# Performance work log

Measured on AMD Instinct MI355X. Metric: run time of the kernel, lower is better.

Reference implementation:

```python
import jax, jax.numpy as jnp
import numpy as np

B, K, E, L, H, ENS = 32768, 5, 16, 128, 3, 3

def setup_inputs() -> dict:
    key = jax.random.key(0)
    ks = jax.random.split(key, 16)
    w = lambda i, shape: (jax.random.normal(ks[i], shape, jnp.float32) * 0.05)
    return {
        "z": jax.random.normal(ks[0], (B, L), jnp.float32),
        "anchors": jax.random.normal(ks[1], (B, K, 2), jnp.float32),
        # anchor_embed MLP: Linear(2,E) -> ReLU -> Linear(E,E)
        "W1": w(2, (E, 2)), "b1": w(3, (E,)),
        "W2": w(4, (E, E)), "b2": w(5, (E,)),
        # LSTMCell(E, L): gates order i,f,g,o
        "W_ih": w(6, (4 * L, E)), "W_hh": w(7, (4 * L, L)),
        "b_ih": w(8, (4 * L,)), "b_hh": w(9, (4 * L,)),
        # progress head Linear(L,1)
        "Wp": w(10, (1, L)), "bp": w(11, (1,)),
        # risk ensemble: ENS stacked Linear(L,1)
        "Wr": w(12, (ENS, L)), "br": w(13, (ENS,)),
    }

def reference(z, anchors, W1, b1, W2, b2, W_ih, W_hh, b_ih, b_hh, Wp, bp, Wr, br):
    Bc, Kc, _ = anchors.shape
    # anchor embedding MLP (B,K,2) -> (B,K,E)
    emb = jnp.maximum(anchors @ W1.T + b1, 0.0) @ W2.T + b2
    inp = emb.reshape(Bc * Kc, -1)                      # (B*K, E)
    h = jnp.broadcast_to(z[:, None, :], (Bc, Kc, z.shape[-1])).reshape(Bc * Kc, -1)
    c = jnp.zeros_like(h)
    x_proj = inp @ W_ih.T + b_ih                        # input projection constant over steps
    for _ in range(H):  # fixed small rollout horizon
        gates = x_proj + h @ W_hh.T + b_hh              # (B*K, 4L)
        i_g, f_g, g_g, o_g = jnp.split(gates, 4, axis=-1)
        i_g = jax.nn.sigmoid(i_g)
        f_g = jax.nn.sigmoid(f_g)
        g_g = jnp.tanh(g_g)
        o_g = jax.nn.sigmoid(o_g)
        c = f_g * c + i_g * g_g
        h = o_g * jnp.tanh(c)
    h = h.reshape(Bc, Kc, -1)                           # (B,K,L)
    progress = (h @ Wp.T + bp)[..., 0]                  # (B,K)
    risks = jnp.einsum('bkl,el->ebk', h, Wr) + br[:, None, None]  # (ENS,B,K)
    risk_mean = risks.mean(axis=0)
    unc = jnp.var(jax.nn.sigmoid(risks), axis=0, ddof=1)  # torch .var is unbiased
    return risk_mean, progress, unc, risks
```

## Files before the change

### kernel.cpp

```cpp
#include <hip/hip_runtime.h>

#define BN 32768
#define KN 5
#define LN 128
#define EN 16
#define HN 3
#define ROWS (BN*KN)
#define BK (BN*KN)
#define MT 32
#define TILES (ROWS/MT)
#define WGS 512
#define TPW (TILES/WGS)
#define THREADS 512
#define ASTR 168
#define HSTR 132

using bf16x8 = __attribute__((ext_vector_type(8))) __bf16;
using f32x4  = __attribute__((ext_vector_type(4))) float;
using u16x8  = __attribute__((ext_vector_type(8))) unsigned short;

__device__ inline unsigned short f2bf(float x) {
    union { float f; unsigned u; } v; v.f = x;
    unsigned r = v.u + 0x7FFFu + ((v.u >> 16) & 1u);
    return (unsigned short)(r >> 16);
}
__device__ inline float sigm(float x) {
    return __builtin_amdgcn_rcpf(1.0f + __builtin_amdgcn_exp2f(-1.44269504089f * x));
}
__device__ inline float tanh_(float x) {
    return 1.0f - 2.0f * __builtin_amdgcn_rcpf(1.0f + __builtin_amdgcn_exp2f(2.88539008178f * x));
}
__device__ inline f32x4 splat4(float x) { f32x4 r; r[0]=x; r[1]=x; r[2]=x; r[3]=x; return r; }

__global__ __launch_bounds__(THREADS, 2)
void wahead_kernel(const float* __restrict__ z,   const float* __restrict__ anchors,
                   const float* __restrict__ W1,  const float* __restrict__ b1,
                   const float* __restrict__ W2,  const float* __restrict__ b2,
                   const float* __restrict__ Wih, const float* __restrict__ Whh,
                   const float* __restrict__ bih, const float* __restrict__ bhh,
                   const float* __restrict__ Wp,  const float* __restrict__ bp,
                   const float* __restrict__ Wr,  const float* __restrict__ br,
                   float* __restrict__ out)
{
    __shared__ unsigned short sA[2 * MT * ASTR];
    __shared__ float sHf[MT * HSTR];
    __shared__ float sW1[32], sb1[16], sW2[256], sb2[16], sWp[128], sWr[384];

    const int tid  = threadIdx.x;
    const int wv   = tid >> 6;
    const int lane = tid & 63;
    const int quad = lane >> 4;
    const int cc   = lane & 15;

    if (tid < 32)  sW1[tid] = W1[tid];
    if (tid < 16)  { sb1[tid] = b1[tid]; sb2[tid] = b2[tid]; }
    if (tid < 256) sW2[tid] = W2[tid];
    if (tid < 128) sWp[tid] = Wp[tid];
    if (tid < 384) sWr[tid] = Wr[tid];

    bf16x8 Bf[4][5];
    float biasv[4];
    #pragma unroll
    for (int t = 0; t < 4; ++t) {
        const int n = t * 128 + wv * 16 + cc;
        biasv[t] = bih[n] + bhh[n];
        #pragma unroll
        for (int kt = 0; kt < 5; ++kt) {
            const int k0 = kt * 32 + quad * 8;
            float v[8];
            if (k0 < 16) {
                const float4 p0 = *reinterpret_cast<const float4*>(Wih + n * 16 + k0);
                const float4 p1 = *reinterpret_cast<const float4*>(Wih + n * 16 + k0 + 4);
                v[0]=p0.x; v[1]=p0.y; v[2]=p0.z; v[3]=p0.w;
                v[4]=p1.x; v[5]=p1.y; v[6]=p1.z; v[7]=p1.w;
            } else if (k0 < 144) {
                const float4 p0 = *reinterpret_cast<const float4*>(Whh + n * 128 + (k0 - 16));
                const float4 p1 = *reinterpret_cast<const float4*>(Whh + n * 128 + (k0 - 16) + 4);
                v[0]=p0.x; v[1]=p0.y; v[2]=p0.z; v[3]=p0.w;
                v[4]=p1.x; v[5]=p1.y; v[6]=p1.z; v[7]=p1.w;
            } else {
                #pragma unroll
                for (int j = 0; j < 8; ++j) v[j] = 0.0f;
            }
            union { bf16x8 bv; unsigned short us[8]; } pk;
            #pragma unroll
            for (int j = 0; j < 8; ++j) pk.us[j] = f2bf(v[j]);
            Bf[t][kt] = pk.bv;
        }
    }

    const float bpv = bp[0];
    const float br0 = br[0], br1 = br[1], br2 = br[2];

    __syncthreads();

    const int erow = tid >> 4;
    const int esub = tid & 15;

    for (int ti = 0; ti < TPW; ++ti) {
        const int tile = blockIdx.x * TPW + ti;
        const int r0g  = tile * MT;

        {
            const int gr = r0g + erow;
            const float ax = anchors[gr * 2], ay = anchors[gr * 2 + 1];
            float acc_e = sb2[esub];
            #pragma unroll
            for (int hh = 0; hh < 16; ++hh) {
                float pre = fmaf(sW1[hh * 2], ax, fmaf(sW1[hh * 2 + 1], ay, sb1[hh]));
                pre = fmaxf(pre, 0.0f);
                acc_e = fmaf(pre, sW2[esub * 16 + hh], acc_e);
            }
            const unsigned short eb = f2bf(acc_e);
            sA[0 * MT * ASTR + erow * ASTR + esub] = eb;
            sA[1 * MT * ASTR + erow * ASTR + esub] = eb;
            sA[0 * MT * ASTR + erow * ASTR + 144 + esub] = 0;
            sA[1 * MT * ASTR + erow * ASTR + 144 + esub] = 0;
            const unsigned b_idx = (unsigned)gr / 5u;
            const float4* zp = reinterpret_cast<const float4*>(z + (size_t)b_idx * 128 + esub * 8);
            const float4 z0 = zp[0], z1 = zp[1];
            union { u16x8 v; unsigned short us[8]; } zz;
            zz.us[0]=f2bf(z0.x); zz.us[1]=f2bf(z0.y); zz.us[2]=f2bf(z0.z); zz.us[3]=f2bf(z0.w);
            zz.us[4]=f2bf(z1.x); zz.us[5]=f2bf(z1.y); zz.us[6]=f2bf(z1.z); zz.us[7]=f2bf(z1.w);
            *reinterpret_cast<u16x8*>(&sA[0 * MT * ASTR + erow * ASTR + 16 + esub * 8]) = zz.v;
        }

        float cst[2][4] = {{0,0,0,0},{0,0,0,0}};

        #pragma unroll
        for (int s = 0; s < HN; ++s) {
            const int cur = s & 1;
            const int nxt = cur ^ 1;
            __syncthreads();

            f32x4 acc[2][4];
            #pragma unroll
            for (int mt = 0; mt < 2; ++mt)
                #pragma unroll
                for (int t = 0; t < 4; ++t)
                    acc[mt][t] = splat4(biasv[t]);

            #pragma unroll
            for (int kt = 0; kt < 5; ++kt) {
                const bf16x8 a0 = *reinterpret_cast<const bf16x8*>(
                    &sA[cur * MT * ASTR + cc * ASTR + kt * 32 + quad * 8]);
                const bf16x8 a1 = *reinterpret_cast<const bf16x8*>(
                    &sA[cur * MT * ASTR + (16 + cc) * ASTR + kt * 32 + quad * 8]);
                #pragma unroll
                for (int t = 0; t < 4; ++t) {
                    acc[0][t] = __builtin_amdgcn_mfma_f32_16x16x32_bf16(a0, Bf[t][kt], acc[0][t], 0, 0, 0);
                    acc[1][t] = __builtin_amdgcn_mfma_f32_16x16x32_bf16(a1, Bf[t][kt], acc[1][t], 0, 0, 0);
                }
            }

            const int lcol = wv * 16 + cc;
            #pragma unroll
            for (int mt = 0; mt < 2; ++mt) {
                #pragma unroll
                for (int r = 0; r < 4; ++r) {
                    const float ig = sigm(acc[mt][0][r]);
                    const float fg = sigm(acc[mt][1][r]);
                    const float gg = tanh_(acc[mt][2][r]);
                    const float og = sigm(acc[mt][3][r]);
                    const float cn = fmaf(fg, cst[mt][r], ig * gg);
                    cst[mt][r] = cn;
                    const float hn = og * tanh_(cn);
                    const int m = mt * 16 + quad * 4 + r;
                    if (s == HN - 1) {
                        sHf[m * HSTR + lcol] = hn;
                    } else {
                        sA[nxt * MT * ASTR + m * ASTR + 16 + lcol] = f2bf(hn);
                    }
                }
            }
        }

        __syncthreads();

        {
            const int row = tid >> 4;
            const int j   = tid & 15;
            float p = 0.f, q0 = 0.f, q1 = 0.f, q2 = 0.f;
            #pragma unroll
            for (int u = 0; u < 8; ++u) {
                const int l = j * 8 + u;
                const float hv = sHf[row * HSTR + l];
                p  = fmaf(hv, sWp[l], p);
                q0 = fmaf(hv, sWr[l], q0);
                q1 = fmaf(hv, sWr[128 + l], q1);
                q2 = fmaf(hv, sWr[256 + l], q2);
            }
            #pragma unroll
            for (int m = 1; m < 16; m <<= 1) {
                p  += __shfl_xor(p,  m, 64);
                q0 += __shfl_xor(q0, m, 64);
                q1 += __shfl_xor(q1, m, 64);
                q2 += __shfl_xor(q2, m, 64);
            }
            if (j == 0) {
                const int gr = r0g + row;
                const float prog  = p + bpv;
                const float rr0 = q0 + br0, rr1 = q1 + br1, rr2 = q2 + br2;
                const float rmean = (rr0 + rr1 + rr2) * (1.0f / 3.0f);
                const float s0 = sigm(rr0), s1 = sigm(rr1), s2 = sigm(rr2);
                const float sm = (s0 + s1 + s2) * (1.0f / 3.0f);
                const float d0 = s0 - sm, d1 = s1 - sm, d2 = s2 - sm;
                const float unc = (d0 * d0 + d1 * d1 + d2 * d2) * 0.5f;
                out[gr]          = rmean;
                out[BK + gr]     = prog;
                out[2 * BK + gr] = unc;
                out[3 * BK + gr] = rr0;
                out[4 * BK + gr] = rr1;
                out[5 * BK + gr] = rr2;
            }
        }
    }
}

extern "C" void kernel_launch(void* const* d_in, const int* in_sizes, int n_in,
                              void* d_out, int out_size, void* d_ws, size_t ws_size,
                              hipStream_t stream) {
    const float* z       = (const float*)d_in[0];
    const float* anchors = (const float*)d_in[1];
    const float* W1      = (const float*)d_in[2];
    const float* b1      = (const float*)d_in[3];
    const float* W2      = (const float*)d_in[4];
    const float* b2      = (const float*)d_in[5];
    const float* Wih     = (const float*)d_in[6];
    const float* Whh     = (const float*)d_in[7];
    const float* bih     = (const float*)d_in[8];
    const float* bhh     = (const float*)d_in[9];
    const float* Wp      = (const float*)d_in[10];
    const float* bp      = (const float*)d_in[11];
    const float* Wr      = (const float*)d_in[12];
    const float* br      = (const float*)d_in[13];

    hipLaunchKernelGGL(wahead_kernel, dim3(WGS), dim3(THREADS), 0, stream,
                       z, anchors, W1, b1, W2, b2, Wih, Whh, bih, bhh,
                       Wp, bp, Wr, br, (float*)d_out);
}
```

Baseline: 236.6 us.

## Trim K padding with a 16-wide MFMA tail and store final h as bf16

Measured after the change: 413.2 us. 74.6% more time.

```diff
diff --git a/kernel.cpp b/kernel.cpp
--- a/kernel.cpp
+++ b/kernel.cpp
@@ -9,21 +9,30 @@
 #define BK (BN*KN)
 #define MT 32
 #define TILES (ROWS/MT)
-#define WGS 512
+#define WGS 1024
 #define TPW (TILES/WGS)
 #define THREADS 512
-#define ASTR 168
-#define HSTR 132
+#define ASTR 152
 
 using bf16x8 = __attribute__((ext_vector_type(8))) __bf16;
 using f32x4  = __attribute__((ext_vector_type(4))) float;
 using u16x8  = __attribute__((ext_vector_type(8))) unsigned short;
+using s16x4  = __attribute__((ext_vector_type(4))) short;
+
+#if __has_builtin(__builtin_amdgcn_mfma_f32_16x16x16bf16_1k)
+#define HAVE_B16K16 1
+#else
+#define HAVE_B16K16 0
+#endif
 
 __device__ inline unsigned short f2bf(float x) {
     union { float f; unsigned u; } v; v.f = x;
     unsigned r = v.u + 0x7FFFu + ((v.u >> 16) & 1u);
     return (unsigned short)(r >> 16);
 }
+__device__ inline float bf2f(unsigned short b) {
+    union { unsigned u; float f; } v; v.u = ((unsigned)b) << 16; return v.f;
+}
 __device__ inline float sigm(float x) {
     return __builtin_amdgcn_rcpf(1.0f + __builtin_amdgcn_exp2f(-1.44269504089f * x));
 }
@@ -32,7 +41,7 @@
 }
 __device__ inline f32x4 splat4(float x) { f32x4 r; r[0]=x; r[1]=x; r[2]=x; r[3]=x; return r; }
 
-__global__ __launch_bounds__(THREADS, 2)
+__global__ __launch_bounds__(THREADS, 4)
 void wahead_kernel(const float* __restrict__ z,   const float* __restrict__ anchors,
                    const float* __restrict__ W1,  const float* __restrict__ b1,
                    const float* __restrict__ W2,  const float* __restrict__ b2,
@@ -43,8 +52,7 @@
                    float* __restrict__ out)
 {
     __shared__ unsigned short sA[2 * MT * ASTR];
-    __shared__ float sHf[MT * HSTR];
-    __shared__ float sW1[32], sb1[16], sW2[256], sb2[16], sWp[128], sWr[384];
+    __shared__ float sW1[32], sb1[16], sW2[16 * 17], sb2[16], sWp[128], sWr[384];
 
     const int tid  = threadIdx.x;
     const int wv   = tid >> 6;
@@ -54,18 +62,23 @@
 
     if (tid < 32)  sW1[tid] = W1[tid];
     if (tid < 16)  { sb1[tid] = b1[tid]; sb2[tid] = b2[tid]; }
-    if (tid < 256) sW2[tid] = W2[tid];
+    if (tid < 256) sW2[(tid >> 4) * 17 + (tid & 15)] = W2[tid];
     if (tid < 128) sWp[tid] = Wp[tid];
     if (tid < 384) sWr[tid] = Wr[tid];
 
-    bf16x8 Bf[4][5];
+    bf16x8 Bf[4][4];
+#if HAVE_B16K16
+    s16x4  B4[4];
+#else
+    bf16x8 B4[4];
+#endif
     float biasv[4];
     #pragma unroll
     for (int t = 0; t < 4; ++t) {
         const int n = t * 128 + wv * 16 + cc;
         biasv[t] = bih[n] + bhh[n];
         #pragma unroll
-        for (int kt = 0; kt < 5; ++kt) {
+        for (int kt = 0; kt < 4; ++kt) {
             const int k0 = kt * 32 + quad * 8;
             float v[8];
             if (k0 < 16) {
@@ -73,20 +86,36 @@
                 const float4 p1 = *reinterpret_cast<const float4*>(Wih + n * 16 + k0 + 4);
                 v[0]=p0.x; v[1]=p0.y; v[2]=p0.z; v[3]=p0.w;
                 v[4]=p1.x; v[5]=p1.y; v[6]=p1.z; v[7]=p1.w;
-            } else if (k0 < 144) {
+            } else {
                 const float4 p0 = *reinterpret_cast<const float4*>(Whh + n * 128 + (k0 - 16));
                 const float4 p1 = *reinterpret_cast<const float4*>(Whh + n * 128 + (k0 - 16) + 4);
                 v[0]=p0.x; v[1]=p0.y; v[2]=p0.z; v[3]=p0.w;
                 v[4]=p1.x; v[5]=p1.y; v[6]=p1.z; v[7]=p1.w;
-            } else {
-                #pragma unroll
-                for (int j = 0; j < 8; ++j) v[j] = 0.0f;
             }
             union { bf16x8 bv; unsigned short us[8]; } pk;
             #pragma unroll
             for (int j = 0; j < 8; ++j) pk.us[j] = f2bf(v[j]);
             Bf[t][kt] = pk.bv;
         }
+#if HAVE_B16K16
+        {
+            const float4 p = *reinterpret_cast<const float4*>(Whh + n * 128 + 112 + quad * 4);
+            union { s16x4 sv; unsigned short us[4]; } pk;
+            pk.us[0]=f2bf(p.x); pk.us[1]=f2bf(p.y); pk.us[2]=f2bf(p.z); pk.us[3]=f2bf(p.w);
+            B4[t] = pk.sv;
+        }
+#else
+        {
+            const int k0 = 128 + quad * 8;
+            union { bf16x8 bv; unsigned short us[8]; } pk;
+            #pragma unroll
+            for (int j = 0; j < 8; ++j) {
+                const int ks = k0 + j;
+                pk.us[j] = (ks < 144) ? f2bf(Whh[n * 128 + (ks - 16)]) : (unsigned short)0;
+            }
+            B4[t] = pk.bv;
+        }
+#endif
     }
 
     const float bpv = bp[0];
@@ -109,13 +138,11 @@
             for (int hh = 0; hh < 16; ++hh) {
                 float pre = fmaf(sW1[hh * 2], ax, fmaf(sW1[hh * 2 + 1], ay, sb1[hh]));
                 pre = fmaxf(pre, 0.0f);
-                acc_e = fmaf(pre, sW2[esub * 16 + hh], acc_e);
+                acc_e = fmaf(pre, sW2[esub * 17 + hh], acc_e);
             }
             const unsigned short eb = f2bf(acc_e);
             sA[0 * MT * ASTR + erow * ASTR + esub] = eb;
             sA[1 * MT * ASTR + erow * ASTR + esub] = eb;
-            sA[0 * MT * ASTR + erow * ASTR + 144 + esub] = 0;
-            sA[1 * MT * ASTR + erow * ASTR + 144 + esub] = 0;
             const unsigned b_idx = (unsigned)gr / 5u;
             const float4* zp = reinterpret_cast<const float4*>(z + (size_t)b_idx * 128 + esub * 8);
             const float4 z0 = zp[0], z1 = zp[1];
@@ -141,7 +168,7 @@
                     acc[mt][t] = splat4(biasv[t]);
 
             #pragma unroll
-            for (int kt = 0; kt < 5; ++kt) {
+            for (int kt = 0; kt < 4; ++kt) {
                 const bf16x8 a0 = *reinterpret_cast<const bf16x8*>(
                     &sA[cur * MT * ASTR + cc * ASTR + kt * 32 + quad * 8]);
                 const bf16x8 a1 = *reinterpret_cast<const bf16x8*>(
@@ -151,6 +178,31 @@
                     acc[0][t] = __builtin_amdgcn_mfma_f32_16x16x32_bf16(a0, Bf[t][kt], acc[0][t], 0, 0, 0);
                     acc[1][t] = __builtin_amdgcn_mfma_f32_16x16x32_bf16(a1, Bf[t][kt], acc[1][t], 0, 0, 0);
                 }
+            }
+            {
+#if HAVE_B16K16
+                const s16x4 a0 = *reinterpret_cast<const s16x4*>(
+                    &sA[cur * MT * ASTR + cc * ASTR + 128 + quad * 4]);
+                const s16x4 a1 = *reinterpret_cast<const s16x4*>(
+                    &sA[cur * MT * ASTR + (16 + cc) * ASTR + 128 + quad * 4]);
+                #pragma unroll
+                for (int t = 0; t < 4; ++t) {
+                    acc[0][t] = __builtin_amdgcn_mfma_f32_16x16x16bf16_1k(a0, B4[t], acc[0][t], 0, 0, 0);
+                    acc[1][t] = __builtin_amdgcn_mfma_f32_16x16x16bf16_1k(a1, B4[t], acc[1][t], 0, 0, 0);
+                }
+#else
+                union { bf16x8 bv; s16x4 lo; unsigned long long hi_zero[2]; } ua0, ua1;
+                ua0.hi_zero[1] = 0; ua1.hi_zero[1] = 0;
+                ua0.lo = *reinterpret_cast<const s16x4*>(
+                    &sA[cur * MT * ASTR + cc * ASTR + 128 + quad * 8]);
+                ua1.lo = *reinterpret_cast<const s16x4*>(
+                    &sA[cur * MT * ASTR + (16 + cc) * ASTR + 128 + quad * 8]);
+                #pragma unroll
+                for (int t = 0; t < 4; ++t) {
+                    acc[0][t] = __builtin_amdgcn_mfma_f32_16x16x32_bf16(ua0.bv, B4[t], acc[0][t], 0, 0, 0);
+                    acc[1][t] = __builtin_amdgcn_mfma_f32_16x16x32_bf16(ua1.bv, B4[t], acc[1][t], 0, 0, 0);
+                }
+#endif
             }
 
             const int lcol = wv * 16 + cc;
@@ -166,11 +218,7 @@
                     cst[mt][r] = cn;
                     const float hn = og * tanh_(cn);
                     const int m = mt * 16 + quad * 4 + r;
-                    if (s == HN - 1) {
-                        sHf[m * HSTR + lcol] = hn;
-                    } else {
-                        sA[nxt * MT * ASTR + m * ASTR + 16 + lcol] = f2bf(hn);
-                    }
+                    sA[nxt * MT * ASTR + m * ASTR + 16 + lcol] = f2bf(hn);
                 }
             }
         }
@@ -180,11 +228,13 @@
         {
             const int row = tid >> 4;
             const int j   = tid & 15;
+            const u16x8 hv8 = *reinterpret_cast<const u16x8*>(
+                &sA[1 * MT * ASTR + row * ASTR + 16 + j * 8]);
             float p = 0.f, q0 = 0.f, q1 = 0.f, q2 = 0.f;
             #pragma unroll
             for (int u = 0; u < 8; ++u) {
                 const int l = j * 8 + u;
-                const float hv = sHf[row * HSTR + l];
+                const float hv = bf2f(hv8[u]);
                 p  = fmaf(hv, sWp[l], p);
                 q0 = fmaf(hv, sWr[l], q0);
                 q1 = fmaf(hv, sWr[128 + l], q1);
```

## Hoist LSTM input projection out of the recurrent loop and shrink LDS footprint

Applied to the files above, without the earlier changes.

Result: slower. 270.8 us (+14.4%).

```diff
diff --git a/kernel.cpp b/kernel.cpp
--- a/kernel.cpp
+++ b/kernel.cpp
@@ -3,27 +3,31 @@
 #define BN 32768
 #define KN 5
 #define LN 128
-#define EN 16
 #define HN 3
 #define ROWS (BN*KN)
-#define BK (BN*KN)
+#define BK ROWS
 #define MT 32
 #define TILES (ROWS/MT)
 #define WGS 512
 #define TPW (TILES/WGS)
 #define THREADS 512
-#define ASTR 168
-#define HSTR 132
+#define HSTR 136
+#define ESTR 40
+#define XSTR 36
 
 using bf16x8 = __attribute__((ext_vector_type(8))) __bf16;
 using f32x4  = __attribute__((ext_vector_type(4))) float;
 using u16x8  = __attribute__((ext_vector_type(8))) unsigned short;
+using u16x4  = __attribute__((ext_vector_type(4))) unsigned short;
 
 __device__ inline unsigned short f2bf(float x) {
     union { float f; unsigned u; } v; v.f = x;
     unsigned r = v.u + 0x7FFFu + ((v.u >> 16) & 1u);
     return (unsigned short)(r >> 16);
 }
+__device__ inline float bf2f(unsigned short b) {
+    union { unsigned u; float f; } v; v.u = ((unsigned)b) << 16; return v.f;
+}
 __device__ inline float sigm(float x) {
     return __builtin_amdgcn_rcpf(1.0f + __builtin_amdgcn_exp2f(-1.44269504089f * x));
 }
@@ -32,7 +36,7 @@
 }
 __device__ inline f32x4 splat4(float x) { f32x4 r; r[0]=x; r[1]=x; r[2]=x; r[3]=x; return r; }
 
-__global__ __launch_bounds__(THREADS, 2)
+__global__ __launch_bounds__(THREADS, 4)
 void wahead_kernel(const float* __restrict__ z,   const float* __restrict__ anchors,
                    const float* __restrict__ W1,  const float* __restrict__ b1,
                    const float* __restrict__ W2,  const float* __restrict__ b2,
@@ -42,9 +46,10 @@
                    const float* __restrict__ Wr,  const float* __restrict__ br,
                    float* __restrict__ out)
 {
-    __shared__ unsigned short sA[2 * MT * ASTR];
-    __shared__ float sHf[MT * HSTR];
-    __shared__ float sW1[32], sb1[16], sW2[256], sb2[16], sWp[128], sWr[384];
+    __shared__ unsigned short sH[2 * MT * HSTR];
+    __shared__ unsigned short sE[MT * ESTR];
+    __shared__ unsigned short sXP[512 * XSTR];
+    __shared__ float sW1[32], sb1[16], sW2[16 * 17], sb2[16], sWp[128], sWr[384];
 
     const int tid  = threadIdx.x;
     const int wv   = tid >> 6;
@@ -54,38 +59,39 @@
 
     if (tid < 32)  sW1[tid] = W1[tid];
     if (tid < 16)  { sb1[tid] = b1[tid]; sb2[tid] = b2[tid]; }
-    if (tid < 256) sW2[tid] = W2[tid];
+    if (tid < 256) sW2[(tid >> 4) * 17 + (tid & 15)] = W2[tid];
     if (tid < 128) sWp[tid] = Wp[tid];
     if (tid < 384) sWr[tid] = Wr[tid];
 
-    bf16x8 Bf[4][5];
-    float biasv[4];
+    bf16x8 Bh[4][4];
+    bf16x8 Bi[4];
+    float  biasv[4];
     #pragma unroll
     for (int t = 0; t < 4; ++t) {
         const int n = t * 128 + wv * 16 + cc;
         biasv[t] = bih[n] + bhh[n];
         #pragma unroll
-        for (int kt = 0; kt < 5; ++kt) {
+        for (int kt = 0; kt < 4; ++kt) {
             const int k0 = kt * 32 + quad * 8;
-            float v[8];
-            if (k0 < 16) {
-                const float4 p0 = *reinterpret_cast<const float4*>(Wih + n * 16 + k0);
-                const float4 p1 = *reinterpret_cast<const float4*>(Wih + n * 16 + k0 + 4);
-                v[0]=p0.x; v[1]=p0.y; v[2]=p0.z; v[3]=p0.w;
-                v[4]=p1.x; v[5]=p1.y; v[6]=p1.z; v[7]=p1.w;
-            } else if (k0 < 144) {
-                const float4 p0 = *reinterpret_cast<const float4*>(Whh + n * 128 + (k0 - 16));
-                const float4 p1 = *reinterpret_cast<const float4*>(Whh + n * 128 + (k0 - 16) + 4);
-                v[0]=p0.x; v[1]=p0.y; v[2]=p0.z; v[3]=p0.w;
-                v[4]=p1.x; v[5]=p1.y; v[6]=p1.z; v[7]=p1.w;
+            const float4 p0 = *reinterpret_cast<const float4*>(Whh + n * 128 + k0);
+            const float4 p1 = *reinterpret_cast<const float4*>(Whh + n * 128 + k0 + 4);
+            union { bf16x8 bv; unsigned short us[8]; } pk;
+            pk.us[0]=f2bf(p0.x); pk.us[1]=f2bf(p0.y); pk.us[2]=f2bf(p0.z); pk.us[3]=f2bf(p0.w);
+            pk.us[4]=f2bf(p1.x); pk.us[5]=f2bf(p1.y); pk.us[6]=f2bf(p1.z); pk.us[7]=f2bf(p1.w);
+            Bh[t][kt] = pk.bv;
+        }
+        {
+            union { bf16x8 bv; unsigned short us[8]; } pk;
+            if (quad < 2) {
+                const float4 p0 = *reinterpret_cast<const float4*>(Wih + n * 16 + quad * 8);
+                const float4 p1 = *reinterpret_cast<const float4*>(Wih + n * 16 + quad * 8 + 4);
+                pk.us[0]=f2bf(p0.x); pk.us[1]=f2bf(p0.y); pk.us[2]=f2bf(p0.z); pk.us[3]=f2bf(p0.w);
+                pk.us[4]=f2bf(p1.x); pk.us[5]=f2bf(p1.y); pk.us[6]=f2bf(p1.z); pk.us[7]=f2bf(p1.w);
             } else {
                 #pragma unroll
-                for (int j = 0; j < 8; ++j) v[j] = 0.0f;
-            }
-            union { bf16x8 bv; unsigned short us[8]; } pk;
-            #pragma unroll
-            for (int j = 0; j < 8; ++j) pk.us[j] = f2bf(v[j]);
-            Bf[t][kt] = pk.bv;
+                for (int j = 0; j < 8; ++j) pk.us[j] = 0;
+            }
+            Bi[t] = pk.bv;
         }
     }
 
@@ -109,20 +115,34 @@
             for (int hh = 0; hh < 16; ++hh) {
                 float pre = fmaf(sW1[hh * 2], ax, fmaf(sW1[hh * 2 + 1], ay, sb1[hh]));
                 pre = fmaxf(pre, 0.0f);
-                acc_e = fmaf(pre, sW2[esub * 16 + hh], acc_e);
-            }
-            const unsigned short eb = f2bf(acc_e);
-            sA[0 * MT * ASTR + erow * ASTR + esub] = eb;
-            sA[1 * MT * ASTR + erow * ASTR + esub] = eb;
-            sA[0 * MT * ASTR + erow * ASTR + 144 + esub] = 0;
-            sA[1 * MT * ASTR + erow * ASTR + 144 + esub] = 0;
+                acc_e = fmaf(pre, sW2[esub * 17 + hh], acc_e);
+            }
+            sE[erow * ESTR + esub]      = f2bf(acc_e);
+            sE[erow * ESTR + 16 + esub] = 0;
             const unsigned b_idx = (unsigned)gr / 5u;
             const float4* zp = reinterpret_cast<const float4*>(z + (size_t)b_idx * 128 + esub * 8);
             const float4 z0 = zp[0], z1 = zp[1];
             union { u16x8 v; unsigned short us[8]; } zz;
             zz.us[0]=f2bf(z0.x); zz.us[1]=f2bf(z0.y); zz.us[2]=f2bf(z0.z); zz.us[3]=f2bf(z0.w);
             zz.us[4]=f2bf(z1.x); zz.us[5]=f2bf(z1.y); zz.us[6]=f2bf(z1.z); zz.us[7]=f2bf(z1.w);
-            *reinterpret_cast<u16x8*>(&sA[0 * MT * ASTR + erow * ASTR + 16 + esub * 8]) = zz.v;
+            *reinterpret_cast<u16x8*>(&sH[erow * HSTR + esub * 8]) = zz.v;
+        }
+
+        __syncthreads();
+
+        #pragma unroll
+        for (int mt = 0; mt < 2; ++mt) {
+            const bf16x8 ae = *reinterpret_cast<const bf16x8*>(&sE[(mt * 16 + cc) * ESTR + quad * 8]);
+            #pragma unroll
+            for (int t = 0; t < 4; ++t) {
+                f32x4 xa = splat4(biasv[t]);
+                xa = __builtin_amdgcn_mfma_f32_16x16x32_bf16(ae, Bi[t], xa, 0, 0, 0);
+                union { u16x4 v; unsigned short us[4]; } pk;
+                #pragma unroll
+                for (int r = 0; r < 4; ++r) pk.us[r] = f2bf(xa[r]);
+                const int n = t * 128 + wv * 16 + cc;
+                *reinterpret_cast<u16x4*>(&sXP[n * XSTR + mt * 16 + quad * 4]) = pk.v;
+            }
         }
 
         float cst[2][4] = {{0,0,0,0},{0,0,0,0}};
@@ -133,44 +153,37 @@
             const int nxt = cur ^ 1;
             __syncthreads();
 
-            f32x4 acc[2][4];
-            #pragma unroll
-            for (int mt = 0; mt < 2; ++mt)
-                #pragma unroll
-                for (int t = 0; t < 4; ++t)
-                    acc[mt][t] = splat4(biasv[t]);
-
-            #pragma unroll
-            for (int kt = 0; kt < 5; ++kt) {
-                const bf16x8 a0 = *reinterpret_cast<const bf16x8*>(
-                    &sA[cur * MT * ASTR + cc * ASTR + kt * 32 + quad * 8]);
-                const bf16x8 a1 = *reinterpret_cast<const bf16x8*>(
-                    &sA[cur * MT * ASTR + (16 + cc) * ASTR + kt * 32 + quad * 8]);
+            #pragma unroll
+            for (int mt = 0; mt < 2; ++mt) {
+                f32x4 acc[4];
                 #pragma unroll
                 for (int t = 0; t < 4; ++t) {
-                    acc[0][t] = __builtin_amdgcn_mfma_f32_16x16x32_bf16(a0, Bf[t][kt], acc[0][t], 0, 0, 0);
-                    acc[1][t] = __builtin_amdgcn_mfma_f32_16x16x32_bf16(a1, Bf[t][kt], acc[1][t], 0, 0, 0);
+                    const int n = t * 128 + wv * 16 + cc;
+                    const u16x4 xv = *reinterpret_cast<const u16x4*>(
+                        &sXP[n * XSTR + mt * 16 + quad * 4]);
+                    #pragma unroll
+                    for (int r = 0; r < 4; ++r) acc[t][r] = bf2f(xv[r]);
                 }
-            }
-
-            const int lcol = wv * 16 + cc;
-            #pragma unroll
-            for (int mt = 0; mt < 2; ++mt) {
+                #pragma unroll
+                for (int kt = 0; kt < 4; ++kt) {
+                    const bf16x8 a = *reinterpret_cast<const bf16x8*>(
+                        &sH[cur * MT * HSTR + (mt * 16 + cc) * HSTR + kt * 32 + quad * 8]);
+                    #pragma unroll
+                    for (int t = 0; t < 4; ++t)
+                        acc[t] = __builtin_amdgcn_mfma_f32_16x16x32_bf16(a, Bh[t][kt], acc[t], 0, 0, 0);
+                }
+                const int lcol = wv * 16 + cc;
                 #pragma unroll
                 for (int r = 0; r < 4; ++r) {
-                    const float ig = sigm(acc[mt][0][r]);
-                    const float fg = sigm(acc[mt][1][r]);
-                    const float gg = tanh_(acc[mt][2][r]);
-                    const float og = sigm(acc[mt][3][r]);
+                    const float ig = sigm(acc[0][r]);
+                    const float fg = sigm(acc[1][r]);
+                    const float gg = tanh_(acc[2][r]);
+                    const float og = sigm(acc[3][r]);
                     const float cn = fmaf(fg, cst[mt][r], ig * gg);
                     cst[mt][r] = cn;
                     const float hn = og * tanh_(cn);
                     const int m = mt * 16 + quad * 4 + r;
-                    if (s == HN - 1) {
-                        sHf[m * HSTR + lcol] = hn;
-                    } else {
-                        sA[nxt * MT * ASTR + m * ASTR + 16 + lcol] = f2bf(hn);
-                    }
+                    sH[nxt * MT * HSTR + m * HSTR + lcol] = f2bf(hn);
                 }
             }
         }
@@ -180,11 +193,13 @@
         {
             const int row = tid >> 4;
             const int j   = tid & 15;
+            const u16x8 hv8 = *reinterpret_cast<const u16x8*>(
+                &sH[1 * MT * HSTR + row * HSTR + j * 8]);
             float p = 0.f, q0 = 0.f, q1 = 0.f, q2 = 0.f;
             #pragma unroll
             for (int u = 0; u < 8; ++u) {
                 const int l = j * 8 + u;
-                const float hv = sHf[row * HSTR + l];
+                const float hv = bf2f(hv8[u]);
                 p  = fmaf(hv, sWp[l], p);
                 q0 = fmaf(hv, sWr[l], q0);
                 q1 = fmaf(hv, sWr[128 + l], q1);
```

## Double row tile to 64 and store final hidden state as bf16 in LDS

Applied to the files above, without the earlier changes.

Result: faster. 230.9 us (-2.4%).

```diff
diff --git a/kernel.cpp b/kernel.cpp
--- a/kernel.cpp
+++ b/kernel.cpp
@@ -3,17 +3,15 @@
 #define BN 32768
 #define KN 5
 #define LN 128
-#define EN 16
 #define HN 3
 #define ROWS (BN*KN)
-#define BK (BN*KN)
-#define MT 32
+#define BK ROWS
+#define MT 64
 #define TILES (ROWS/MT)
 #define WGS 512
 #define TPW (TILES/WGS)
 #define THREADS 512
 #define ASTR 168
-#define HSTR 132
 
 using bf16x8 = __attribute__((ext_vector_type(8))) __bf16;
 using f32x4  = __attribute__((ext_vector_type(4))) float;
@@ -23,6 +21,9 @@
     union { float f; unsigned u; } v; v.f = x;
     unsigned r = v.u + 0x7FFFu + ((v.u >> 16) & 1u);
     return (unsigned short)(r >> 16);
+}
+__device__ inline float bf2f(unsigned short b) {
+    union { unsigned u; float f; } v; v.u = ((unsigned)b) << 16; return v.f;
 }
 __device__ inline float sigm(float x) {
     return __builtin_amdgcn_rcpf(1.0f + __builtin_amdgcn_exp2f(-1.44269504089f * x));
@@ -43,8 +44,7 @@
                    float* __restrict__ out)
 {
     __shared__ unsigned short sA[2 * MT * ASTR];
-    __shared__ float sHf[MT * HSTR];
-    __shared__ float sW1[32], sb1[16], sW2[256], sb2[16], sWp[128], sWr[384];
+    __shared__ float sW1[32], sb1[16], sW2[16 * 17], sb2[16], sWp[128], sWr[384];
 
     const int tid  = threadIdx.x;
     const int wv   = tid >> 6;
@@ -54,12 +54,12 @@
 
     if (tid < 32)  sW1[tid] = W1[tid];
     if (tid < 16)  { sb1[tid] = b1[tid]; sb2[tid] = b2[tid]; }
-    if (tid < 256) sW2[tid] = W2[tid];
+    if (tid < 256) sW2[(tid >> 4) * 17 + (tid & 15)] = W2[tid];
     if (tid < 128) sWp[tid] = Wp[tid];
     if (tid < 384) sWr[tid] = Wr[tid];
 
     bf16x8 Bf[4][5];
-    float biasv[4];
+    float  biasv[4];
     #pragma unroll
     for (int t = 0; t < 4; ++t) {
         const int n = t * 128 + wv * 16 + cc;
@@ -94,8 +94,8 @@
 
     __syncthreads();
 
-    const int erow = tid >> 4;
-    const int esub = tid & 15;
+    const int erow = tid >> 3;
+    const int esub = tid & 7;
 
     for (int ti = 0; ti < TPW; ++ti) {
         const int tile = blockIdx.x * TPW + ti;
@@ -104,28 +104,36 @@
         {
             const int gr = r0g + erow;
             const float ax = anchors[gr * 2], ay = anchors[gr * 2 + 1];
-            float acc_e = sb2[esub];
+            const int e0 = esub * 2;
+            float a0 = sb2[e0], a1 = sb2[e0 + 1];
             #pragma unroll
             for (int hh = 0; hh < 16; ++hh) {
                 float pre = fmaf(sW1[hh * 2], ax, fmaf(sW1[hh * 2 + 1], ay, sb1[hh]));
                 pre = fmaxf(pre, 0.0f);
-                acc_e = fmaf(pre, sW2[esub * 16 + hh], acc_e);
-            }
-            const unsigned short eb = f2bf(acc_e);
-            sA[0 * MT * ASTR + erow * ASTR + esub] = eb;
-            sA[1 * MT * ASTR + erow * ASTR + esub] = eb;
-            sA[0 * MT * ASTR + erow * ASTR + 144 + esub] = 0;
-            sA[1 * MT * ASTR + erow * ASTR + 144 + esub] = 0;
+                a0 = fmaf(pre, sW2[e0 * 17 + hh], a0);
+                a1 = fmaf(pre, sW2[(e0 + 1) * 17 + hh], a1);
+            }
+            const unsigned short b0 = f2bf(a0), b1v = f2bf(a1);
+            #pragma unroll
+            for (int bufi = 0; bufi < 2; ++bufi) {
+                unsigned short* row = &sA[bufi * MT * ASTR + erow * ASTR];
+                row[e0]     = b0;  row[e0 + 1]     = b1v;
+                row[144 + e0] = 0; row[144 + e0 + 1] = 0;
+            }
             const unsigned b_idx = (unsigned)gr / 5u;
-            const float4* zp = reinterpret_cast<const float4*>(z + (size_t)b_idx * 128 + esub * 8);
-            const float4 z0 = zp[0], z1 = zp[1];
-            union { u16x8 v; unsigned short us[8]; } zz;
-            zz.us[0]=f2bf(z0.x); zz.us[1]=f2bf(z0.y); zz.us[2]=f2bf(z0.z); zz.us[3]=f2bf(z0.w);
-            zz.us[4]=f2bf(z1.x); zz.us[5]=f2bf(z1.y); zz.us[6]=f2bf(z1.z); zz.us[7]=f2bf(z1.w);
-            *reinterpret_cast<u16x8*>(&sA[0 * MT * ASTR + erow * ASTR + 16 + esub * 8]) = zz.v;
-        }
-
-        float cst[2][4] = {{0,0,0,0},{0,0,0,0}};
+            const float4* zp = reinterpret_cast<const float4*>(z + (size_t)b_idx * 128 + esub * 16);
+            const float4 z0 = zp[0], z1 = zp[1], z2 = zp[2], z3 = zp[3];
+            union { u16x8 v; unsigned short us[8]; } w0, w1;
+            w0.us[0]=f2bf(z0.x); w0.us[1]=f2bf(z0.y); w0.us[2]=f2bf(z0.z); w0.us[3]=f2bf(z0.w);
+            w0.us[4]=f2bf(z1.x); w0.us[5]=f2bf(z1.y); w0.us[6]=f2bf(z1.z); w0.us[7]=f2bf(z1.w);
+            w1.us[0]=f2bf(z2.x); w1.us[1]=f2bf(z2.y); w1.us[2]=f2bf(z2.z); w1.us[3]=f2bf(z2.w);
+            w1.us[4]=f2bf(z3.x); w1.us[5]=f2bf(z3.y); w1.us[6]=f2bf(z3.z); w1.us[7]=f2bf(z3.w);
+            unsigned short* hrow = &sA[erow * ASTR + 16 + esub * 16];
+            *reinterpret_cast<u16x8*>(hrow)     = w0.v;
+            *reinterpret_cast<u16x8*>(hrow + 8) = w1.v;
+        }
+
+        float cst[4][4] = {{0,0,0,0},{0,0,0,0},{0,0,0,0},{0,0,0,0}};
 
         #pragma unroll
         for (int s = 0; s < HN; ++s) {
@@ -133,44 +141,32 @@
             const int nxt = cur ^ 1;
             __syncthreads();
 
-            f32x4 acc[2][4];
-            #pragma unroll
-            for (int mt = 0; mt < 2; ++mt)
-                #pragma unroll
-                for (int t = 0; t < 4; ++t)
-                    acc[mt][t] = splat4(biasv[t]);
-
-            #pragma unroll
-            for (int kt = 0; kt < 5; ++kt) {
-                const bf16x8 a0 = *reinterpret_cast<const bf16x8*>(
-                    &sA[cur * MT * ASTR + cc * ASTR + kt * 32 + quad * 8]);
-                const bf16x8 a1 = *reinterpret_cast<const bf16x8*>(
-                    &sA[cur * MT * ASTR + (16 + cc) * ASTR + kt * 32 + quad * 8]);
-                #pragma unroll
-                for (int t = 0; t < 4; ++t) {
-                    acc[0][t] = __builtin_amdgcn_mfma_f32_16x16x32_bf16(a0, Bf[t][kt], acc[0][t], 0, 0, 0);
-                    acc[1][t] = __builtin_amdgcn_mfma_f32_16x16x32_bf16(a1, Bf[t][kt], acc[1][t], 0, 0, 0);
+            #pragma unroll
+            for (int mt = 0; mt < 4; ++mt) {
+                f32x4 acc[4];
+                #pragma unroll
+                for (int t = 0; t < 4; ++t) acc[t] = splat4(biasv[t]);
+
+                #pragma unroll
+                for (int kt = 0; kt < 5; ++kt) {
+                    const bf16x8 a = *reinterpret_cast<const bf16x8*>(
+                        &sA[cur * MT * ASTR + (mt * 16 + cc) * ASTR + kt * 32 + quad * 8]);
+                    #pragma unroll
+                    for (int t = 0; t < 4; ++t)
+                        acc[t] = __builtin_amdgcn_mfma_f32_16x16x32_bf16(a, Bf[t][kt], acc[t], 0, 0, 0);
                 }
-            }
-
-            const int lcol = wv * 16 + cc;
-            #pragma unroll
-            for (int mt = 0; mt < 2; ++mt) {
+                const int lcol = wv * 16 + cc;
                 #pragma unroll
                 for (int r = 0; r < 4; ++r) {
-                    const float ig = sigm(acc[mt][0][r]);
-                    const float fg = sigm(acc[mt][1][r]);
-                    const float gg = tanh_(acc[mt][2][r]);
-                    const float og = sigm(acc[mt][3][r]);
+                    const float ig = sigm(acc[0][r]);
+                    const float fg = sigm(acc[1][r]);
+                    const float gg = tanh_(acc[2][r]);
+                    const float og = sigm(acc[3][r]);
                     const float cn = fmaf(fg, cst[mt][r], ig * gg);
                     cst[mt][r] = cn;
                     const float hn = og * tanh_(cn);
                     const int m = mt * 16 + quad * 4 + r;
-                    if (s == HN - 1) {
-                        sHf[m * HSTR + lcol] = hn;
-                    } else {
-                        sA[nxt * MT * ASTR + m * ASTR + 16 + lcol] = f2bf(hn);
-                    }
+                    sA[nxt * MT * ASTR + m * ASTR + 16 + lcol] = f2bf(hn);
                 }
             }
         }
@@ -178,20 +174,23 @@
         __syncthreads();
 
         {
-            const int row = tid >> 4;
-            const int j   = tid & 15;
+            const int row = tid >> 3;
+            const int j   = tid & 7;
+            const unsigned short* hrow = &sA[1 * MT * ASTR + row * ASTR + 16 + j * 16];
+            const u16x8 h0 = *reinterpret_cast<const u16x8*>(hrow);
+            const u16x8 h1 = *reinterpret_cast<const u16x8*>(hrow + 8);
             float p = 0.f, q0 = 0.f, q1 = 0.f, q2 = 0.f;
             #pragma unroll
-            for (int u = 0; u < 8; ++u) {
-                const int l = j * 8 + u;
-                const float hv = sHf[row * HSTR + l];
+            for (int u = 0; u < 16; ++u) {
+                const int l = j * 16 + u;
+                const float hv = bf2f(u < 8 ? h0[u] : h1[u - 8]);
                 p  = fmaf(hv, sWp[l], p);
                 q0 = fmaf(hv, sWr[l], q0);
                 q1 = fmaf(hv, sWr[128 + l], q1);
                 q2 = fmaf(hv, sWr[256 + l], q2);
             }
             #pragma unroll
-            for (int m = 1; m < 16; m <<= 1) {
+            for (int m = 1; m < 8; m <<= 1) {
                 p  += __shfl_xor(p,  m, 64);
                 q0 += __shfl_xor(q0, m, 64);
                 q1 += __shfl_xor(q1, m, 64);
```
